# Performance work log

Measured on AMD Instinct MI355X. Metric: run time of the kernel, lower is better.

The kernel has to match this reference:

```python
import jax, jax.numpy as jnp
import numpy as np

N, LQ, LK, D, H = 2, 2048, 2048, 1024, 16


def setup_inputs() -> dict:
    root = jax.random.key(0)
    k0, k1, k2, k3, k4 = jax.random.split(root, 5)
    s = 1.0 / np.float32(np.sqrt(D))  # fan-in init scale for Linear weights
    query = jax.random.normal(k0, (N, LQ, D), jnp.float32)
    key = jax.random.normal(k1, (N, LK, D), jnp.float32)
    Wq = jax.random.normal(k2, (D, D), jnp.float32) * s
    Wk = jax.random.normal(k3, (D, D), jnp.float32) * s
    Wv = jax.random.normal(k4, (D, D), jnp.float32) * s
    # causal mask: True above the diagonal => attention set to -inf
    mask = jnp.triu(jnp.ones((LQ, LK), dtype=bool), k=1)
    # padding mask: per-sentence valid key lengths (tail is padding)
    lengths = jnp.array([LK, LK - 256], dtype=jnp.int32)  # (N,)
    padding_mask = jnp.arange(LK)[None, :] >= lengths[:, None]  # (N, LK) bool
    return {"query": query, "key": key, "Wq": Wq, "Wk": Wk, "Wv": Wv,
            "mask": mask, "padding_mask": padding_mask, "n_heads": H}


def reference(query, key, Wq, Wk, Wv, mask, padding_mask, n_heads):
    n, lq, d_model = query.shape
    lk = key.shape[1]
    h = n_heads
    d = d_model // h
    # torch Linear: y = x @ W^T  (no bias)
    q = (query @ Wq.T).reshape(n, lq, h, d).transpose(0, 2, 1, 3)  # (N,H,Lq,d)
    k = (key @ Wk.T).reshape(n, lk, h, d).transpose(0, 2, 1, 3)    # (N,H,Lk,d)
    v = (key @ Wv.T).reshape(n, lk, h, d).transpose(0, 2, 1, 3)    # (N,H,Lk,d)
    # non-standard scaling: sqrt of the number of valid (non-padded) keys per sentence
    valid = jnp.sum((~padding_mask).astype(q.dtype), axis=-1)      # (N,)
    scaling = jnp.sqrt(valid)[:, None, None, None]                 # (N,1,1,1)
    score = jnp.einsum('nhqd,nhkd->nhqk', q, k) / scaling          # (N,H,Lq,Lk)
    full_mask = mask[None, None, :, :] | padding_mask[:, None, None, :]
    score = jnp.where(full_mask, -jnp.inf, score)
    p = jax.nn.softmax(score, axis=-1)
    attn = jnp.einsum('nhqk,nhkd->nhqd', p, v)                     # (N,H,Lq,d)
    return attn.transpose(0, 2, 1, 3).reshape(n, lq, d_model)
```

## Files before the change

### kernel.cpp

```cpp
#include <hip/hip_runtime.h>
#include <math.h>

typedef __attribute__((ext_vector_type(8))) short short8;
typedef __attribute__((ext_vector_type(4))) float f32x4;

#define NB 2
#define LQ 2048
#define LK 2048
#define DM 1024
#define NH 16
#define HD 64

__device__ __forceinline__ unsigned short f2bf(float f) {
    unsigned u = __builtin_bit_cast(unsigned, f);
    u = (u + 0x7FFFu + ((u >> 16) & 1u)) >> 16;
    return (unsigned short)u;
}

__device__ __forceinline__ void gload16(const void* g, void* l) {
    __builtin_amdgcn_global_load_lds(
        (const __attribute__((address_space(1))) void*)g,
        (__attribute__((address_space(3))) void*)l, 16, 0, 0);
}

__device__ __forceinline__ unsigned cvtpk(float a, float b) {
    unsigned r;
    asm("v_cvt_pk_bf16_f32 %0, %1, %2" : "=v"(r) : "v"(a), "v"(b));
    return r;
}

__device__ __forceinline__ short8 lds_load8(const unsigned short* base, int row, int col) {
    int byte = (row * 128 + col * 2) ^ ((row & 7) << 4);
    return *(const short8*)((const char*)base + byte);
}

__device__ __forceinline__ short8 lds32(const unsigned short* base, int row, int col) {
    int byte = (row * 64 + col * 2) ^ ((row & 3) << 4);
    return *(const short8*)((const char*)base + byte);
}

__global__ __launch_bounds__(256) void convertk(
    const float* __restrict__ q, const float* __restrict__ k,
    const float* __restrict__ wq, const float* __restrict__ wk,
    const float* __restrict__ wv, unsigned short* __restrict__ dst)
{
    long i4 = (long)blockIdx.x * 256 + threadIdx.x;
    long e = i4 * 4;
    if (e >= 11534336L) return;
    const float* src; long off;
    if (e < 4194304L)       { src = q;  off = e; }
    else if (e < 8388608L)  { src = k;  off = e - 4194304L; }
    else if (e < 9437184L)  { src = wq; off = e - 8388608L; }
    else if (e < 10485760L) { src = wk; off = e - 9437184L; }
    else                    { src = wv; off = e - 10485760L; }
    float4 v = *(const float4*)(src + off);
    ushort4 r;
    r.x = f2bf(v.x); r.y = f2bf(v.y); r.z = f2bf(v.z); r.w = f2bf(v.w);
    *(ushort4*)(dst + e) = r;
}

__device__ __forceinline__ void gemm_stage(
    const unsigned short* A, const unsigned short* B,
    unsigned short* As, unsigned short* Bs,
    int bm, int bn, int k0, int wave, int srow, int scol)
{
    const int K = DM;
    int i0 = wave, i1 = wave + 4;
    gload16(A + (size_t)(bm + i0 * 16 + srow) * K + k0 + scol, As + i0 * 512);
    gload16(B + (size_t)(bn + i0 * 16 + srow) * K + k0 + scol, Bs + i0 * 512);
    gload16(A + (size_t)(bm + i1 * 16 + srow) * K + k0 + scol, As + i1 * 512);
    gload16(B + (size_t)(bn + i1 * 16 + srow) * K + k0 + scol, Bs + i1 * 512);
}

__global__ __launch_bounds__(256) void gemm3(
    const unsigned short* __restrict__ Qb, const unsigned short* __restrict__ Kb,
    const unsigned short* __restrict__ Wqb, const unsigned short* __restrict__ Wkb,
    const unsigned short* __restrict__ Wvb,
    unsigned short* __restrict__ Qp, unsigned short* __restrict__ Kp, unsigned short* __restrict__ Vp)
{
    const unsigned short *A, *B;
    unsigned short* C;
    int z = blockIdx.z;
    if (z == 0)      { A = Qb; B = Wqb; C = Qp; }
    else if (z == 1) { A = Kb; B = Wkb; C = Kp; }
    else             { A = Kb; B = Wvb; C = Vp; }
    const int NN = DM;
    __shared__ unsigned short As[2][4096];
    __shared__ unsigned short Bs[2][4096];
    int t = threadIdx.x, wave = t >> 6, lane = t & 63;
    int bm = blockIdx.x * 128, bn = blockIdx.y * 128;
    int wr = (wave >> 1) * 64, wc = (wave & 1) * 64;
    int srow = lane >> 2;
    int scol = ((lane & 3) ^ (srow & 3)) << 3;
    int frow = lane & 15, fk = (lane >> 4) * 8;
    f32x4 zero = {0.f, 0.f, 0.f, 0.f};
    f32x4 acc[4][4];
    for (int i = 0; i < 4; i++) for (int j = 0; j < 4; j++) acc[i][j] = zero;

    gemm_stage(A, B, As[0], Bs[0], bm, bn, 0, wave, srow, scol);
    __syncthreads();
    for (int s = 0; s < 32; s++) {
        int cur = s & 1;
        if (s + 1 < 32)
            gemm_stage(A, B, As[cur ^ 1], Bs[cur ^ 1], bm, bn, (s + 1) * 32, wave, srow, scol);
        short8 af[4], bfr[4];
#pragma unroll
        for (int i = 0; i < 4; i++) af[i]  = lds32(As[cur], wr + i * 16 + frow, fk);
#pragma unroll
        for (int j = 0; j < 4; j++) bfr[j] = lds32(Bs[cur], wc + j * 16 + frow, fk);
#pragma unroll
        for (int i = 0; i < 4; i++)
#pragma unroll
            for (int j = 0; j < 4; j++)
                acc[i][j] = __builtin_amdgcn_mfma_f32_16x16x32_bf16(af[i], bfr[j], acc[i][j], 0, 0, 0);
        __syncthreads();
    }
    int ccol = lane & 15, crow = (lane >> 4) * 4;
#pragma unroll
    for (int i = 0; i < 4; i++)
#pragma unroll
        for (int j = 0; j < 4; j++) {
            int col = bn + wc + j * 16 + ccol;
#pragma unroll
            for (int r = 0; r < 4; r++) {
                int row = bm + wr + i * 16 + crow + r;
                C[(size_t)row * NN + col] = f2bf(acc[i][j][r]);
            }
        }
}

__global__ __launch_bounds__(256) void transposek(const unsigned short* __restrict__ V,
                                                  unsigned short* __restrict__ Vt)
{
    __shared__ unsigned short tile[64][65];
    int n = blockIdx.z;
    int k0 = blockIdx.x * 64, d0 = blockIdx.y * 64;
    int t = threadIdx.x;
#pragma unroll
    for (int it = 0; it < 2; it++) {
        int r = (t >> 3) + it * 32, c = (t & 7) * 8;
        short8 v = *(const short8*)&V[((size_t)(n * LK + k0 + r)) * DM + d0 + c];
#pragma unroll
        for (int j = 0; j < 8; j++) tile[r][c + j] = (unsigned short)v[j];
    }
    __syncthreads();
#pragma unroll
    for (int it = 0; it < 2; it++) {
        int r2 = (t >> 3) + it * 32, c2 = (t & 7) * 8;
        short8 v;
#pragma unroll
        for (int j = 0; j < 8; j++) v[j] = (short)tile[c2 + j][r2];
        *(short8*)&Vt[((size_t)(n * DM + d0 + r2)) * LK + k0 + c2] = v;
    }
}


__device__ __forceinline__ void stage_kv64(
    const unsigned short* Kbase, const unsigned short* Vbase,
    unsigned short* KsB, unsigned short* VsB,
    int k0, int w, int srl, int scs)
{
#pragma unroll
    for (int ii = 0; ii < 2; ii++) {
        int r0 = (w + 4 * ii) * 8;
        gload16(Kbase + (size_t)(k0 + r0 + srl) * DM + scs, KsB + r0 * 64);
        gload16(Vbase + (size_t)(r0 + srl) * LK + k0 + scs, VsB + r0 * 64);
    }
}

__device__ __forceinline__ void softmax_pack(
    f32x4 (&sv)[4], unsigned short* PsW,
    int qw, int k0, int vlen, float c2,
    f32x4 (&o)[4], float& m_run, float& l_run, int lane)
{
    const int c = lane & 15, g = lane >> 4;
    bool full = (k0 + 63 <= qw) && (k0 + 64 <= vlen);
    if (!full) {
        int q = qw + c;
#pragma unroll
        for (int kt = 0; kt < 4; kt++)
#pragma unroll
            for (int r = 0; r < 4; r++) {
                int kg = k0 + kt * 16 + g * 4 + r;
                if (kg > q || kg >= vlen) sv[kt][r] = -INFINITY;
            }
    }
    float mx = fmaxf(fmaxf(sv[0][0], sv[0][1]), fmaxf(sv[0][2], sv[0][3]));
#pragma unroll
    for (int kt = 1; kt < 4; kt++)
        mx = fmaxf(mx, fmaxf(fmaxf(sv[kt][0], sv[kt][1]), fmaxf(sv[kt][2], sv[kt][3])));
    mx = fmaxf(mx, __shfl_xor(mx, 16));
    mx = fmaxf(mx, __shfl_xor(mx, 32));
    if (__any((mx - m_run) * c2 > 8.0f)) {
        float mn = fmaxf(m_run, mx);
        float al = __builtin_amdgcn_exp2f((m_run - mn) * c2);
        float alr[4];
#pragma unroll
        for (int r = 0; r < 4; r++) alr[r] = __shfl(al, 4 * g + r);
#pragma unroll
        for (int dt = 0; dt < 4; dt++)
#pragma unroll
            for (int r = 0; r < 4; r++) o[dt][r] *= alr[r];
        l_run *= al;
        m_run = mn;
    }
    float ssum = 0.f;
#pragma unroll
    for (int kt = 0; kt < 4; kt++)
#pragma unroll
        for (int r = 0; r < 4; r++) {
            float p = __builtin_amdgcn_exp2f((sv[kt][r] - m_run) * c2);
            sv[kt][r] = p;
            ssum += p;
        }
    ssum += __shfl_xor(ssum, 16);
    ssum += __shfl_xor(ssum, 32);
    l_run += ssum;
#pragma unroll
    for (int kt = 0; kt < 4; kt++) {
        uint2 pw;
        pw.x = cvtpk(sv[kt][0], sv[kt][1]);
        pw.y = cvtpk(sv[kt][2], sv[kt][3]);
        int byte = (c * 128 + (kt * 16 + g * 4) * 2) ^ ((c & 7) << 4);
        *(uint2*)((char*)PsW + byte) = pw;
    }
}

__device__ __forceinline__ void attn_epilogue(float* out, const f32x4 (&o)[4], float l_run,
                                              int n, int h, int qw, int c, int g)
{
    float lr[4];
#pragma unroll
    for (int r = 0; r < 4; r++) lr[r] = __shfl(l_run, 4 * g + r);
#pragma unroll
    for (int dt = 0; dt < 4; dt++)
#pragma unroll
        for (int r = 0; r < 4; r++) {
            int q = qw + 4 * g + r;
            int d = h * HD + dt * 16 + c;
            out[((size_t)n * LQ + q) * DM + d] = o[dt][r] / lr[r];
        }
}

__global__ __launch_bounds__(256, 4) void attnk(
    const unsigned short* __restrict__ Qp, const unsigned short* __restrict__ Kp,
    const unsigned short* __restrict__ Vt, const unsigned char* __restrict__ pm,
    float* __restrict__ out)
{
    __shared__ unsigned short Ks[2][4096];
    __shared__ unsigned short Vs[2][4096];
    __shared__ unsigned short Ps[4][1024];
    int t = threadIdx.x, w = t >> 6, lane = t & 63;
    int bid = blockIdx.x;
    int nh = (bid & 7) * 4 + ((bid >> 3) & 3);
    int n = nh >> 4, h = nh & 15;
    int jj = (bid >> 5) & 7, rr = bid >> 8;
    int qc = (rr == 0) ? 31 - jj : (rr == 1) ? 16 + jj : (rr == 2) ? 15 - jj : jj;
    int qw = qc * 64 + 16 * w;
    const int c = lane & 15, g = lane >> 4, fk = g * 8;

    int vlen;
    {
        const uint4* pmv = (const uint4*)(pm + (size_t)n * LK);
        uint4 a = pmv[lane * 2], b = pmv[lane * 2 + 1];
        int ones = __popc(a.x) + __popc(a.y) + __popc(a.z) + __popc(a.w)
                 + __popc(b.x) + __popc(b.y) + __popc(b.z) + __popc(b.w);
        int zeros = 32 - ones;
#pragma unroll
        for (int off = 1; off < 64; off <<= 1) zeros += __shfl_xor(zeros, off);
        vlen = zeros;
    }
    float c2 = 1.4426950408889634f / sqrtf((float)vlen);
    int kvt = (vlen + 63) >> 6;
    int nt = min(qc + 1, kvt);

    int srl = lane >> 3;
    int scs = ((lane & 7) ^ srl) << 3;
    const unsigned short* Kbase = Kp + (size_t)n * LK * DM + h * HD;
    const unsigned short* Vbase = Vt + ((size_t)n * DM + h * HD) * LK;

    const unsigned short* qp = Qp + (size_t)(n * LQ + qw + c) * DM + h * HD;
    short8 q0 = *(const short8*)(qp + fk), q1 = *(const short8*)(qp + 32 + fk);

    f32x4 zero = {0.f, 0.f, 0.f, 0.f};
    f32x4 o[4] = {zero, zero, zero, zero};
    float m_run = -INFINITY, l_run = 0.f;
    unsigned short* PsW = Ps[w];

    stage_kv64(Kbase, Vbase, Ks[0], Vs[0], 0, w, srl, scs);
    __syncthreads();

    for (int ti = 0; ti < nt; ti++) {
        int cur = ti & 1, k0 = ti * 64;
        if (ti + 1 < nt)
            stage_kv64(Kbase, Vbase, Ks[cur ^ 1], Vs[cur ^ 1], k0 + 64, w, srl, scs);

        f32x4 sv[4];
        __builtin_amdgcn_s_setprio(1);
#pragma unroll
        for (int kt = 0; kt < 4; kt++) {
            short8 kf0 = lds_load8(Ks[cur], kt * 16 + c, fk);
            short8 kf1 = lds_load8(Ks[cur], kt * 16 + c, 32 + fk);
            f32x4 z = zero;
            z = __builtin_amdgcn_mfma_f32_16x16x32_bf16(kf0, q0, z, 0, 0, 0);
            z = __builtin_amdgcn_mfma_f32_16x16x32_bf16(kf1, q1, z, 0, 0, 0);
            sv[kt] = z;
        }
        __builtin_amdgcn_s_setprio(0);

        softmax_pack(sv, PsW, qw, k0, vlen, c2, o, m_run, l_run, lane);

        __builtin_amdgcn_s_setprio(1);
#pragma unroll
        for (int ks = 0; ks < 2; ks++) {
            short8 ap = lds_load8(PsW, c, ks * 32 + fk);
#pragma unroll
            for (int dt = 0; dt < 4; dt++) {
                short8 bv = lds_load8(Vs[cur], dt * 16 + c, ks * 32 + fk);
                o[dt] = __builtin_amdgcn_mfma_f32_16x16x32_bf16(ap, bv, o[dt], 0, 0, 0);
            }
        }
        __builtin_amdgcn_s_setprio(0);
        __syncthreads();
    }
    attn_epilogue(out, o, l_run, n, h, qw, c, g);
}

extern "C" void kernel_launch(void* const* d_in, const int* in_sizes, int n_in,
                              void* d_out, int out_size, void* d_ws, size_t ws_size,
                              hipStream_t stream) {
    const float* query = (const float*)d_in[0];
    const float* key   = (const float*)d_in[1];
    const float* Wq    = (const float*)d_in[2];
    const float* Wk    = (const float*)d_in[3];
    const float* Wv    = (const float*)d_in[4];
    const unsigned char* pmask = (const unsigned char*)d_in[6];
    float* out = (float*)d_out;

    char* ws = (char*)d_ws;
    unsigned short* bfbase = (unsigned short*)ws;
    unsigned short* Qb  = bfbase;
    unsigned short* Kb  = bfbase + 4194304L;
    unsigned short* Wqb = bfbase + 8388608L;
    unsigned short* Wkb = bfbase + 9437184L;
    unsigned short* Wvb = bfbase + 10485760L;
    unsigned short* Qp  = (unsigned short*)(ws + 23068672L);
    unsigned short* Kp  = (unsigned short*)(ws + 31457280L);
    unsigned short* Vp  = (unsigned short*)(ws + 39845888L);
    unsigned short* Vt  = (unsigned short*)(ws + 48234496L);

    convertk<<<11264, 256, 0, stream>>>(query, key, Wq, Wk, Wv, bfbase);
    gemm3<<<dim3(32, 8, 3), 256, 0, stream>>>(Qb, Kb, Wqb, Wkb, Wvb, Qp, Kp, Vp);
    transposek<<<dim3(32, 16, 2), 256, 0, stream>>>(Vp, Vt);
    attnk<<<1024, 256, 0, stream>>>(Qp, Kp, Vt, pmask, out);
}
```

Baseline: 191.7 us.

## Fuse V transpose into GEMM epilogue, fold scale into Q, MFMA row sums

The V projection GEMM now writes its output directly in transposed layout, which removes the separate transpose kernel and its extra round trip through global memory. In the attention kernel, the softmax scale is folded into Q once at load, so the per-element multiplies in exp2 go away. Row sums are now accumulated with an MFMA against a ones vector instead of shuffle reductions, and the max reduction uses v_max3. The GEMM LDS swizzle is also changed. The risks are an extra bf16 rounding of the scaled Q and scattered 8-byte stores in the transposed epilogue.

```diff
diff --git a/kernel.cpp b/kernel.cpp
--- a/kernel.cpp
+++ b/kernel.cpp
@@ -29,13 +29,19 @@
     return r;
 }
 
+__device__ __forceinline__ float max3f(float a, float b, float c) {
+    float r;
+    asm("v_max3_f32 %0, %1, %2, %3" : "=v"(r) : "v"(a), "v"(b), "v"(c));
+    return r;
+}
+
 __device__ __forceinline__ short8 lds_load8(const unsigned short* base, int row, int col) {
     int byte = (row * 128 + col * 2) ^ ((row & 7) << 4);
     return *(const short8*)((const char*)base + byte);
 }
 
 __device__ __forceinline__ short8 lds32(const unsigned short* base, int row, int col) {
-    int byte = (row * 64 + col * 2) ^ ((row & 3) << 4);
+    int byte = (row * 64 + col * 2) ^ (((row >> 2) & 3) << 4);
     return *(const short8*)((const char*)base + byte);
 }
 
@@ -76,14 +82,13 @@
     const unsigned short* __restrict__ Qb, const unsigned short* __restrict__ Kb,
     const unsigned short* __restrict__ Wqb, const unsigned short* __restrict__ Wkb,
     const unsigned short* __restrict__ Wvb,
-    unsigned short* __restrict__ Qp, unsigned short* __restrict__ Kp, unsigned short* __restrict__ Vp)
+    unsigned short* __restrict__ Qp, unsigned short* __restrict__ Kp, unsigned short* __restrict__ Vt)
 {
     const unsigned short *A, *B;
-    unsigned short* C;
     int z = blockIdx.z;
-    if (z == 0)      { A = Qb; B = Wqb; C = Qp; }
-    else if (z == 1) { A = Kb; B = Wkb; C = Kp; }
-    else             { A = Kb; B = Wvb; C = Vp; }
+    if (z == 0)      { A = Qb; B = Wqb; }
+    else if (z == 1) { A = Kb; B = Wkb; }
+    else             { A = Kb; B = Wvb; }
     const int NN = DM;
     __shared__ unsigned short As[2][4096];
     __shared__ unsigned short Bs[2][4096];
@@ -91,7 +96,7 @@
     int bm = blockIdx.x * 128, bn = blockIdx.y * 128;
     int wr = (wave >> 1) * 64, wc = (wave & 1) * 64;
     int srow = lane >> 2;
-    int scol = ((lane & 3) ^ (srow & 3)) << 3;
+    int scol = ((lane & 3) ^ ((srow >> 2) & 3)) << 3;
     int frow = lane & 15, fk = (lane >> 4) * 8;
     f32x4 zero = {0.f, 0.f, 0.f, 0.f};
     f32x4 acc[4][4];
@@ -116,41 +121,32 @@
         __syncthreads();
     }
     int ccol = lane & 15, crow = (lane >> 4) * 4;
-#pragma unroll
-    for (int i = 0; i < 4; i++)
-#pragma unroll
-        for (int j = 0; j < 4; j++) {
-            int col = bn + wc + j * 16 + ccol;
-#pragma unroll
-            for (int r = 0; r < 4; r++) {
-                int row = bm + wr + i * 16 + crow + r;
-                C[(size_t)row * NN + col] = f2bf(acc[i][j][r]);
+    if (z < 2) {
+        unsigned short* C = (z == 0) ? Qp : Kp;
+#pragma unroll
+        for (int i = 0; i < 4; i++)
+#pragma unroll
+            for (int j = 0; j < 4; j++) {
+                int col = bn + wc + j * 16 + ccol;
+#pragma unroll
+                for (int r = 0; r < 4; r++) {
+                    int row = bm + wr + i * 16 + crow + r;
+                    C[(size_t)row * NN + col] = f2bf(acc[i][j][r]);
+                }
             }
-        }
-}
-
-__global__ __launch_bounds__(256) void transposek(const unsigned short* __restrict__ V,
-                                                  unsigned short* __restrict__ Vt)
-{
-    __shared__ unsigned short tile[64][65];
-    int n = blockIdx.z;
-    int k0 = blockIdx.x * 64, d0 = blockIdx.y * 64;
-    int t = threadIdx.x;
-#pragma unroll
-    for (int it = 0; it < 2; it++) {
-        int r = (t >> 3) + it * 32, c = (t & 7) * 8;
-        short8 v = *(const short8*)&V[((size_t)(n * LK + k0 + r)) * DM + d0 + c];
-#pragma unroll
-        for (int j = 0; j < 8; j++) tile[r][c + j] = (unsigned short)v[j];
-    }
-    __syncthreads();
-#pragma unroll
-    for (int it = 0; it < 2; it++) {
-        int r2 = (t >> 3) + it * 32, c2 = (t & 7) * 8;
-        short8 v;
-#pragma unroll
-        for (int j = 0; j < 8; j++) v[j] = (short)tile[c2 + j][r2];
-        *(short8*)&Vt[((size_t)(n * DM + d0 + r2)) * LK + k0 + c2] = v;
+    } else {
+#pragma unroll
+        for (int i = 0; i < 4; i++)
+#pragma unroll
+            for (int j = 0; j < 4; j++) {
+                int col = bn + wc + j * 16 + ccol;
+                int row0 = bm + wr + i * 16 + crow;
+                int nn = row0 >> 11, l0 = row0 & 2047;
+                ushort4 v4;
+                v4.x = f2bf(acc[i][j][0]); v4.y = f2bf(acc[i][j][1]);
+                v4.z = f2bf(acc[i][j][2]); v4.w = f2bf(acc[i][j][3]);
+                *(ushort4*)&Vt[((size_t)(nn * DM + col)) * LK + l0] = v4;
+            }
     }
 }
 
@@ -170,8 +166,8 @@
 
 __device__ __forceinline__ void softmax_pack(
     f32x4 (&sv)[4], unsigned short* PsW,
-    int qw, int k0, int vlen, float c2,
-    f32x4 (&o)[4], float& m_run, float& l_run, int lane)
+    int qw, int k0, int vlen,
+    f32x4 (&o)[4], f32x4& lsum, float& m_run, int lane)
 {
     const int c = lane & 15, g = lane >> 4;
     bool full = (k0 + 63 <= qw) && (k0 + 64 <= vlen);
@@ -185,15 +181,19 @@
                 if (kg > q || kg >= vlen) sv[kt][r] = -INFINITY;
             }
     }
-    float mx = fmaxf(fmaxf(sv[0][0], sv[0][1]), fmaxf(sv[0][2], sv[0][3]));
-#pragma unroll
-    for (int kt = 1; kt < 4; kt++)
-        mx = fmaxf(mx, fmaxf(fmaxf(sv[kt][0], sv[kt][1]), fmaxf(sv[kt][2], sv[kt][3])));
+    float mx = max3f(sv[0][0], sv[0][1], sv[0][2]);
+    mx = max3f(mx, sv[0][3], sv[1][0]);
+    mx = max3f(mx, sv[1][1], sv[1][2]);
+    mx = max3f(mx, sv[1][3], sv[2][0]);
+    mx = max3f(mx, sv[2][1], sv[2][2]);
+    mx = max3f(mx, sv[2][3], sv[3][0]);
+    mx = max3f(mx, sv[3][1], sv[3][2]);
+    mx = fmaxf(mx, sv[3][3]);
     mx = fmaxf(mx, __shfl_xor(mx, 16));
     mx = fmaxf(mx, __shfl_xor(mx, 32));
-    if (__any((mx - m_run) * c2 > 8.0f)) {
+    if (__any(mx - m_run > 8.0f)) {
         float mn = fmaxf(m_run, mx);
-        float al = __builtin_amdgcn_exp2f((m_run - mn) * c2);
+        float al = __builtin_amdgcn_exp2f(m_run - mn);
         float alr[4];
 #pragma unroll
         for (int r = 0; r < 4; r++) alr[r] = __shfl(al, 4 * g + r);
@@ -201,21 +201,15 @@
         for (int dt = 0; dt < 4; dt++)
 #pragma unroll
             for (int r = 0; r < 4; r++) o[dt][r] *= alr[r];
-        l_run *= al;
+#pragma unroll
+        for (int r = 0; r < 4; r++) lsum[r] *= alr[r];
         m_run = mn;
     }
-    float ssum = 0.f;
 #pragma unroll
     for (int kt = 0; kt < 4; kt++)
 #pragma unroll
-        for (int r = 0; r < 4; r++) {
-            float p = __builtin_amdgcn_exp2f((sv[kt][r] - m_run) * c2);
-            sv[kt][r] = p;
-            ssum += p;
-        }
-    ssum += __shfl_xor(ssum, 16);
-    ssum += __shfl_xor(ssum, 32);
-    l_run += ssum;
+        for (int r = 0; r < 4; r++)
+            sv[kt][r] = __builtin_amdgcn_exp2f(sv[kt][r] - m_run);
 #pragma unroll
     for (int kt = 0; kt < 4; kt++) {
         uint2 pw;
@@ -224,22 +218,6 @@
         int byte = (c * 128 + (kt * 16 + g * 4) * 2) ^ ((c & 7) << 4);
         *(uint2*)((char*)PsW + byte) = pw;
     }
-}
-
-__device__ __forceinline__ void attn_epilogue(float* out, const f32x4 (&o)[4], float l_run,
-                                              int n, int h, int qw, int c, int g)
-{
-    float lr[4];
-#pragma unroll
-    for (int r = 0; r < 4; r++) lr[r] = __shfl(l_run, 4 * g + r);
-#pragma unroll
-    for (int dt = 0; dt < 4; dt++)
-#pragma unroll
-        for (int r = 0; r < 4; r++) {
-            int q = qw + 4 * g + r;
-            int d = h * HD + dt * 16 + c;
-            out[((size_t)n * LQ + q) * DM + d] = o[dt][r] / lr[r];
-        }
 }
 
 __global__ __launch_bounds__(256, 4) void attnk(
@@ -280,11 +258,23 @@
     const unsigned short* Vbase = Vt + ((size_t)n * DM + h * HD) * LK;
 
     const unsigned short* qp = Qp + (size_t)(n * LQ + qw + c) * DM + h * HD;
-    short8 q0 = *(const short8*)(qp + fk), q1 = *(const short8*)(qp + 32 + fk);
+    short8 q0r = *(const short8*)(qp + fk), q1r = *(const short8*)(qp + 32 + fk);
+    short8 q0, q1;
+#pragma unroll
+    for (int j = 0; j < 8; j++) {
+        float f0 = __builtin_bit_cast(float, ((unsigned)(unsigned short)q0r[j]) << 16) * c2;
+        float f1 = __builtin_bit_cast(float, ((unsigned)(unsigned short)q1r[j]) << 16) * c2;
+        q0[j] = (short)f2bf(f0);
+        q1[j] = (short)f2bf(f1);
+    }
+    short8 onesf;
+#pragma unroll
+    for (int j = 0; j < 8; j++) onesf[j] = (short)0x3F80;
 
     f32x4 zero = {0.f, 0.f, 0.f, 0.f};
     f32x4 o[4] = {zero, zero, zero, zero};
-    float m_run = -INFINITY, l_run = 0.f;
+    f32x4 lsum = zero;
+    float m_run = -INFINITY;
     unsigned short* PsW = Ps[w];
 
     stage_kv64(Kbase, Vbase, Ks[0], Vs[0], 0, w, srl, scs);
@@ -308,7 +298,7 @@
         }
         __builtin_amdgcn_s_setprio(0);
 
-        softmax_pack(sv, PsW, qw, k0, vlen, c2, o, m_run, l_run, lane);
+        softmax_pack(sv, PsW, qw, k0, vlen, o, lsum, m_run, lane);
 
         __builtin_amdgcn_s_setprio(1);
 #pragma unroll
@@ -319,11 +309,19 @@
                 short8 bv = lds_load8(Vs[cur], dt * 16 + c, ks * 32 + fk);
                 o[dt] = __builtin_amdgcn_mfma_f32_16x16x32_bf16(ap, bv, o[dt], 0, 0, 0);
             }
+            lsum = __builtin_amdgcn_mfma_f32_16x16x32_bf16(ap, onesf, lsum, 0, 0, 0);
         }
         __builtin_amdgcn_s_setprio(0);
         __syncthreads();
     }
-    attn_epilogue(out, o, l_run, n, h, qw, c, g);
+#pragma unroll
+    for (int dt = 0; dt < 4; dt++)
+#pragma unroll
+        for (int r = 0; r < 4; r++) {
+            int q = qw + 4 * g + r;
+            int d = h * HD + dt * 16 + c;
+            out[((size_t)n * LQ + q) * DM + d] = o[dt][r] / lsum[r];
+        }
 }
 
 extern "C" void kernel_launch(void* const* d_in, const int* in_sizes, int n_in,
@@ -346,11 +344,9 @@
     unsigned short* Wvb = bfbase + 10485760L;
     unsigned short* Qp  = (unsigned short*)(ws + 23068672L);
     unsigned short* Kp  = (unsigned short*)(ws + 31457280L);
-    unsigned short* Vp  = (unsigned short*)(ws + 39845888L);
-    unsigned short* Vt  = (unsigned short*)(ws + 48234496L);
+    unsigned short* Vt  = (unsigned short*)(ws + 39845888L);
 
     convertk<<<11264, 256, 0, stream>>>(query, key, Wq, Wk, Wv, bfbase);
-    gemm3<<<dim3(32, 8, 3), 256, 0, stream>>>(Qb, Kb, Wqb, Wkb, Wvb, Qp, Kp, Vp);
-    transposek<<<dim3(32, 16, 2), 256, 0, stream>>>(Vp, Vt);
+    gemm3<<<dim3(32, 8, 3), 256, 0, stream>>>(Qb, Kb, Wqb, Wkb, Wvb, Qp, Kp, Vt);
     attnk<<<1024, 256, 0, stream>>>(Qp, Kp, Vt, pmask, out);
 }
```

Measured after the change: 201.9 us. 1.05x slower.
